# Optimization experiments

Hardware: AMD Instinct MI355X
Metric: run time of the kernel (lower is better)

Reference implementation:

```python
import jax, jax.numpy as jnp
from jax import lax
import numpy as np

C = 768      # embed_dim
H = 8        # num_heads
SR = 2       # sr_ratio
EPS = 1e-5


def setup_inputs() -> dict:
    key = jax.random.key(0)
    ks = jax.random.split(key, 8)
    B, n = 1, 24
    N = n ** 3  # 13824
    s = 0.02
    x = jax.random.normal(ks[0], (B, N, C), jnp.float32)
    wq = jax.random.normal(ks[1], (C, C), jnp.float32) * s          # query (no bias)
    wkv = jax.random.normal(ks[2], (C, 2 * C), jnp.float32) * s     # key_value (no bias)
    sr_w = jax.random.normal(ks[3], (C, C, SR, SR, SR), jnp.float32) * s  # Conv3d OIDHW
    sr_b = jax.random.normal(ks[4], (C,), jnp.float32) * s
    ln_g = jnp.ones((C,), jnp.float32)
    ln_b = jnp.zeros((C,), jnp.float32)
    proj_w = jax.random.normal(ks[5], (C, C), jnp.float32) * s
    proj_b = jax.random.normal(ks[6], (C,), jnp.float32) * s
    return {"x": x, "wq": wq, "wkv": wkv, "sr_w": sr_w, "sr_b": sr_b,
            "ln_g": ln_g, "ln_b": ln_b, "proj_w": proj_w, "proj_b": proj_b}


def reference(x, wq, wkv, sr_w, sr_b, ln_g, ln_b, proj_w, proj_b):
    B, N, Cdim = x.shape
    d = Cdim // H
    n = round(N ** (1.0 / 3.0))
    # q: [B,H,N,d]
    q = (x @ wq).reshape(B, N, H, d).transpose(0, 2, 1, 3)
    # spatial reduction: conv3d with kernel=stride=SR
    x_ = x.transpose(0, 2, 1).reshape(B, Cdim, n, n, n)
    x_ = lax.conv_general_dilated(x_, sr_w, (SR, SR, SR), 'VALID',
                                  dimension_numbers=('NCDHW', 'OIDHW', 'NCDHW'))
    x_ = x_ + sr_b[None, :, None, None, None]
    x_ = x_.reshape(B, Cdim, -1).transpose(0, 2, 1)  # [B, N', C]
    mu = x_.mean(-1, keepdims=True)
    var = x_.var(-1, keepdims=True)
    x_ = (x_ - mu) / jnp.sqrt(var + EPS) * ln_g + ln_b
    # kv: [2,B,H,N',d]
    kv = (x_ @ wkv).reshape(B, -1, 2, H, d).transpose(2, 0, 3, 1, 4)
    k, v = kv[0], kv[1]
    # NOTE: original scales by sqrt(num_heads), not sqrt(head_dim) -- kept faithfully.
    scores = jnp.einsum('bhqd,bhkd->bhqk', q, k) / jnp.sqrt(jnp.float32(H))
    probs = jax.nn.softmax(scores, axis=-1)
    out = jnp.einsum('bhqk,bhkd->bhqd', probs, v)
    out = out.transpose(0, 2, 1, 3).reshape(B, N, Cdim)
    return out @ proj_w + proj_b
```

## Files before the change

kernel.cpp:

```cpp
#include <hip/hip_runtime.h>
#include <hip/hip_bf16.h>

typedef __hip_bfloat16 bf16;
typedef unsigned short u16;

#define CD 768
#define HH 8
#define HD 96
#define NT 13824
#define NR 1728
#define KCONV 6144

typedef __attribute__((ext_vector_type(8))) __bf16 bf16x8;
typedef __attribute__((ext_vector_type(8))) unsigned short us8;
typedef __attribute__((ext_vector_type(4))) unsigned short us4;
typedef __attribute__((ext_vector_type(4))) float floatx4;

#define OFF_XB   0L
#define OFF_Q    21233664L
#define OFF_XR   42467328L
#define OFF_XLN  47775744L
#define OFF_WQT  50429952L
#define OFF_WKVT 51609600L
#define OFF_PRJT 53968896L
#define OFF_SRWR 55148544L
#define OFF_PRB  64587264L
#define OFF_FLAG 64588800L

__device__ __forceinline__ float b2f(bf16 v) { return __bfloat162float(v); }
__device__ __forceinline__ floatx4 mfma16(bf16x8 a, bf16x8 b, floatx4 c) {
    return __builtin_amdgcn_mfma_f32_16x16x32_bf16(a, b, c, 0, 0, 0);
}
__device__ __forceinline__ u16 f2bf_bits(float x) {
    return __builtin_bit_cast(u16, __float2bfloat16(x));
}
__device__ __forceinline__ float ldin(const void* p, long i, int bf) {
    return bf ? b2f(((const bf16*)p)[i]) : ((const float*)p)[i];
}

__global__ void detect_kernel(const unsigned short* __restrict__ g, int* __restrict__ flag) {
    *flag = (g[0] == 0x3F80) ? 1 : 0;
}

__global__ __launch_bounds__(256) void cvt_kernel(
    const void* __restrict__ src, bf16* __restrict__ dst, long nchunk,
    const int* __restrict__ flagp)
{
    const int bf = *flagp;
    long c = (long)blockIdx.x * 256 + threadIdx.x;
    if (c >= nchunk) return;
    if (bf) {
        ((us8*)dst)[c] = ((const us8*)src)[c];
    } else {
        const float* s = (const float*)src + c * 8;
        us8 o;
#pragma unroll
        for (int j = 0; j < 8; ++j) o[j] = f2bf_bits(s[j]);
        ((us8*)dst)[c] = o;
    }
}

__global__ __launch_bounds__(256) void trans_kernel(
    const void* __restrict__ src, bf16* __restrict__ dst, int R, int Cc,
    const int* __restrict__ flagp)
{
    const int bf = *flagp;
    __shared__ float tile[32][33];
    const int tx = threadIdx.x & 31, ty = threadIdx.x >> 5;
    const int bx = blockIdx.x * 32, by = blockIdx.y * 32;
#pragma unroll
    for (int rr = 0; rr < 4; ++rr)
        tile[ty + rr * 8][tx] = ldin(src, (long)(by + ty + rr * 8) * Cc + bx + tx, bf);
    __syncthreads();
#pragma unroll
    for (int rr = 0; rr < 4; ++rr)
        dst[(long)(bx + ty + rr * 8) * R + by + tx] =
            __float2bfloat16(tile[tx][ty + rr * 8]);
}

__global__ __launch_bounds__(256) void reorder_srw_kernel(
    const void* __restrict__ src, bf16* __restrict__ dst,
    const int* __restrict__ flagp)
{
    const int bf = *flagp;
    const long total = 768L * 6144;
    for (long e = (long)blockIdx.x * 256 + threadIdx.x; e < total;
         e += (long)gridDim.x * 256) {
        long o = e / 6144;
        int rem = (int)(e - o * 6144);
        int tap = rem / 768, i = rem - tap * 768;
        dst[e] = __float2bfloat16(ldin(src, o * 6144 + i * 8 + tap, bf));
    }
}

template <bool GATHER, bool BIAS, int DST, int SPLITK, bool PRESCALE>
__global__ __launch_bounds__(256) void gemm_mfma(
    const bf16* __restrict__ A, const bf16* __restrict__ Bt,
    const bf16* __restrict__ bias, void* __restrict__ C, bf16* __restrict__ C2,
    int M, int N, int K, const int* __restrict__ flagp)
{
    const int bf = (DST == 0) ? *flagp : 0;
    __shared__ u16 Al[128][40];
    __shared__ u16 Bl[128][40];
    const int tid  = threadIdx.x;
    const int wave = tid >> 6, lane = tid & 63;
    const int l15  = lane & 15, quad = lane >> 4;
    const int m0 = blockIdx.y * 128, n0 = blockIdx.x * 128;
    const int mw = (wave & 1) * 64, nw = (wave >> 1) * 64;
    const int srow = tid >> 1, koff = (tid & 1) * 16;

    const int mclamp = min(m0 + srow, M - 1);
    int tokbase = 0;
    if (GATHER) {
        int zo = mclamp / 144, yo = (mclamp / 12) % 12, xo = mclamp % 12;
        tokbase = zo * 1152 + yo * 48 + xo * 2;
    }
    const long arow_off = (long)mclamp * K;
    const long brow_off = (long)(n0 + srow) * K;

    floatx4 acc[4][4];
#pragma unroll
    for (int mi = 0; mi < 4; ++mi)
#pragma unroll
        for (int ni = 0; ni < 4; ++ni) acc[mi][ni] = (floatx4){0.f, 0.f, 0.f, 0.f};

    const int ksteps = K >> 5;
    const int kchunk = ksteps / SPLITK;
    const int kb0 = (SPLITK > 1) ? blockIdx.z * kchunk : 0;
    for (int kb = kb0; kb < kb0 + kchunk; ++kb) {
        const bf16* asrc;
        if (GATHER) {
            int kk0 = kb << 5;
            int tap = kk0 / 768;
            int i0  = kk0 - tap * 768 + koff;
            int tok = tokbase + (tap >> 2) * 576 + ((tap >> 1) & 1) * 24 + (tap & 1);
            asrc = A + (long)tok * 768 + i0;
        } else {
            asrc = A + arow_off + (kb << 5) + koff;
        }
        us8 a0 = *(const us8*)asrc;
        us8 a1 = *(const us8*)(asrc + 8);
        us8 b0 = *(const us8*)(Bt + brow_off + (kb << 5) + koff);
        us8 b1 = *(const us8*)(Bt + brow_off + (kb << 5) + koff + 8);
        __syncthreads();
        *(us8*)&Al[srow][koff]     = a0;
        *(us8*)&Al[srow][koff + 8] = a1;
        *(us8*)&Bl[srow][koff]     = b0;
        *(us8*)&Bl[srow][koff + 8] = b1;
        __syncthreads();

        bf16x8 af[4], bfr[4];
#pragma unroll
        for (int mi = 0; mi < 4; ++mi)
            af[mi] = *(const bf16x8*)&Al[mw + mi * 16 + l15][quad * 8];
#pragma unroll
        for (int ni = 0; ni < 4; ++ni)
            bfr[ni] = *(const bf16x8*)&Bl[nw + ni * 16 + l15][quad * 8];
#pragma unroll
        for (int mi = 0; mi < 4; ++mi)
#pragma unroll
            for (int ni = 0; ni < 4; ++ni)
                acc[mi][ni] = mfma16(af[mi], bfr[ni], acc[mi][ni]);
    }

#pragma unroll
    for (int mi = 0; mi < 4; ++mi) {
        int rowb = m0 + mw + mi * 16 + quad * 4;
#pragma unroll
        for (int ni = 0; ni < 4; ++ni) {
            int col = n0 + nw + ni * 16 + l15;
            float bv = BIAS ? b2f(bias[col]) : 0.f;
#pragma unroll
            for (int r = 0; r < 4; ++r) {
                int row = rowb + r;
                if (row < M) {
                    float v = acc[mi][ni][r] + bv;
                    if (PRESCALE) v *= 0.35355339059327373f;
                    long idx = (long)row * N + col;
                    if (DST == 2)      ((float*)C)[idx] = v;
                    else if (DST == 1) ((bf16*)C)[idx] = __float2bfloat16(v);
                    else if (DST == 3) {
                        if (col < 768) ((bf16*)C)[(long)row * 768 + col] = __float2bfloat16(v);
                        else           C2[(long)(col - 768) * NR + row] = __float2bfloat16(v);
                    } else if (DST == 4) {
                        atomicAdd((float*)C + idx, v);
                    } else {
                        if (bf) ((bf16*)C)[idx] = __float2bfloat16(v);
                        else    ((float*)C)[idx] = v;
                    }
                }
            }
        }
    }
}

__global__ __launch_bounds__(256) void ln_kernel(
    const float* __restrict__ Xr, const void* __restrict__ srb,
    const void* __restrict__ g, const void* __restrict__ b,
    bf16* __restrict__ Xln, const int* __restrict__ flagp)
{
    const int bf = *flagp;
    __shared__ float red[256];
    __shared__ float mu_s, rs_s;
    const int t = blockIdx.x, tid = threadIdx.x;
    const float* row = Xr + (long)t * CD;
    float v0 = row[tid]       + ldin(srb, tid, bf);
    float v1 = row[tid + 256] + ldin(srb, tid + 256, bf);
    float v2 = row[tid + 512] + ldin(srb, tid + 512, bf);
    red[tid] = v0 + v1 + v2;
    __syncthreads();
    for (int off = 128; off; off >>= 1) {
        if (tid < off) red[tid] += red[tid + off];
        __syncthreads();
    }
    if (tid == 0) mu_s = red[0] * (1.0f / CD);
    __syncthreads();
    float mu = mu_s;
    float d0 = v0 - mu, d1 = v1 - mu, d2 = v2 - mu;
    red[tid] = d0 * d0 + d1 * d1 + d2 * d2;
    __syncthreads();
    for (int off = 128; off; off >>= 1) {
        if (tid < off) red[tid] += red[tid + off];
        __syncthreads();
    }
    if (tid == 0) rs_s = rsqrtf(red[0] * (1.0f / CD) + 1e-5f);
    __syncthreads();
    float rs = rs_s;
    bf16* orow = Xln + (long)t * CD;
    orow[tid]       = __float2bfloat16(d0 * rs * ldin(g, tid, bf)       + ldin(b, tid, bf));
    orow[tid + 256] = __float2bfloat16(d1 * rs * ldin(g, tid + 256, bf) + ldin(b, tid + 256, bf));
    orow[tid + 512] = __float2bfloat16(d2 * rs * ldin(g, tid + 512, bf) + ldin(b, tid + 512, bf));
}

__global__ __launch_bounds__(256) void attn_mfma_kernel(
    const bf16* __restrict__ Qg, const bf16* __restrict__ Kg,
    const bf16* __restrict__ VTg, bf16* __restrict__ Og)
{
    __shared__ u16 Ks[64][104];
    __shared__ u16 Vt[96][72];
    __shared__ u16 PT[4][32][72];

    const int tid  = threadIdx.x;
    const int wave = tid >> 6;
    const int lane = tid & 63;
    const int l15  = lane & 15;
    const int quad = lane >> 4;

    const int lin  = blockIdx.y * 108 + blockIdx.x;
    const int nid  = (lin & 7) * 108 + (lin >> 3);
    const int h    = nid / 108;
    const int qblk = nid - h * 108;
    const int q0   = qblk * 128 + wave * 32;

    bf16x8 bq[2][3];
#pragma unroll
    for (int qc = 0; qc < 2; ++qc)
#pragma unroll
        for (int kc = 0; kc < 3; ++kc)
            bq[qc][kc] = *(const bf16x8*)(Qg + (long)(q0 + qc * 16 + l15) * CD
                                          + h * HD + kc * 32 + quad * 8);

    floatx4 o[2][6];
    float lp[2] = {0.f, 0.f};
#pragma unroll
    for (int qc = 0; qc < 2; ++qc)
#pragma unroll
        for (int dc = 0; dc < 6; ++dc) o[qc][dc] = (floatx4){0.f, 0.f, 0.f, 0.f};

    const int stok = tid >> 2;
    const int dseg = (tid & 3) * 24;
    const int vdim = tid >> 3;
    const int vt8  = (tid & 7) << 3;
    const u16* kbase = (const u16*)Kg + (long)stok * 768 + h * HD + dseg;
    const u16* vbase = (const u16*)VTg + (long)(h * HD + vdim) * NR + vt8;

    us8 kreg[3], vreg[3];
#pragma unroll
    for (int s = 0; s < 3; ++s) kreg[s] = *(const us8*)(kbase + s * 8);
#pragma unroll
    for (int i = 0; i < 3; ++i) vreg[i] = *(const us8*)(vbase + (long)i * 32 * NR);

    for (int kt = 0; kt < NR; kt += 64) {
        __syncthreads();
#pragma unroll
        for (int s = 0; s < 3; ++s) *(us8*)&Ks[stok][dseg + s * 8] = kreg[s];
#pragma unroll
        for (int i = 0; i < 3; ++i) *(us8*)&Vt[vdim + i * 32][vt8] = vreg[i];
        __syncthreads();

        if (kt + 64 < NR) {
            const u16* k2 = kbase + (long)(kt + 64) * 768;
            const u16* v2 = vbase + (kt + 64);
#pragma unroll
            for (int s = 0; s < 3; ++s) kreg[s] = *(const us8*)(k2 + s * 8);
#pragma unroll
            for (int i = 0; i < 3; ++i) vreg[i] = *(const us8*)(v2 + (long)i * 32 * NR);
        }

#pragma unroll
        for (int tc = 0; tc < 4; ++tc) {
            bf16x8 ak[3];
#pragma unroll
            for (int kc = 0; kc < 3; ++kc)
                ak[kc] = *(const bf16x8*)&Ks[tc * 16 + l15][kc * 32 + quad * 8];
#pragma unroll
            for (int qc = 0; qc < 2; ++qc) {
                floatx4 acc = {0.f, 0.f, 0.f, 0.f};
#pragma unroll
                for (int kc = 0; kc < 3; ++kc) acc = mfma16(ak[kc], bq[qc][kc], acc);
                float e0 = __expf(acc[0]), e1 = __expf(acc[1]);
                float e2 = __expf(acc[2]), e3 = __expf(acc[3]);
                lp[qc] += (e0 + e1) + (e2 + e3);
                us4 p4;
                p4[0] = f2bf_bits(e0); p4[1] = f2bf_bits(e1);
                p4[2] = f2bf_bits(e2); p4[3] = f2bf_bits(e3);
                *(us4*)&PT[wave][qc * 16 + l15][tc * 16 + quad * 4] = p4;
            }
        }

#pragma unroll
        for (int ks = 0; ks < 2; ++ks) {
            bf16x8 ap[2];
#pragma unroll
            for (int qc = 0; qc < 2; ++qc)
                ap[qc] = *(const bf16x8*)&PT[wave][qc * 16 + l15][ks * 32 + quad * 8];
#pragma unroll
            for (int dc = 0; dc < 6; ++dc) {
                bf16x8 bv = *(const bf16x8*)&Vt[dc * 16 + l15][ks * 32 + quad * 8];
#pragma unroll
                for (int qc = 0; qc < 2; ++qc)
                    o[qc][dc] = mfma16(ap[qc], bv, o[qc][dc]);
            }
        }
    }

#pragma unroll
    for (int qc = 0; qc < 2; ++qc) {
        float ls = lp[qc];
        ls += __shfl_xor(ls, 16);
        ls += __shfl_xor(ls, 32);
        float inv = 1.0f / ls;
#pragma unroll
        for (int r = 0; r < 4; ++r) {
            float invr = __shfl(inv, quad * 4 + r, 16);
            int row = q0 + qc * 16 + quad * 4 + r;
#pragma unroll
            for (int dc = 0; dc < 6; ++dc)
                Og[(long)row * CD + h * HD + dc * 16 + l15] =
                    __float2bfloat16(o[qc][dc][r] * invr);
        }
    }
}

extern "C" void kernel_launch(void* const* d_in, const int* in_sizes, int n_in,
                              void* d_out, int out_size, void* d_ws, size_t ws_size,
                              hipStream_t stream) {
    const void* x      = d_in[0];
    const void* wq     = d_in[1];
    const void* wkv    = d_in[2];
    const void* sr_w   = d_in[3];
    const void* sr_b   = d_in[4];
    const void* ln_g   = d_in[5];
    const void* ln_b   = d_in[6];
    const void* proj_w = d_in[7];
    const void* proj_b = d_in[8];

    char* ws = (char*)d_ws;
    bf16*  xb    = (bf16*)(ws + OFF_XB);
    bf16*  O     = (bf16*)(ws + OFF_XB);
    bf16*  Q     = (bf16*)(ws + OFF_Q);
    float* Xr    = (float*)(ws + OFF_XR);
    bf16*  Kg    = (bf16*)(ws + OFF_XR);
    bf16*  VTg   = (bf16*)(ws + OFF_XR + 2654208);
    bf16*  Xln   = (bf16*)(ws + OFF_XLN);
    bf16*  wqT   = (bf16*)(ws + OFF_WQT);
    bf16*  wkvT  = (bf16*)(ws + OFF_WKVT);
    bf16*  prjT  = (bf16*)(ws + OFF_PRJT);
    bf16*  srwR  = (bf16*)(ws + OFF_SRWR);
    bf16*  prbB  = (bf16*)(ws + OFF_PRB);
    int*   flag  = (int*)(ws + OFF_FLAG);

    detect_kernel<<<1, 1, 0, stream>>>((const unsigned short*)ln_g, flag);
    cvt_kernel<<<5184, 256, 0, stream>>>(x, xb, (long)NT * CD / 8, flag);
    trans_kernel<<<dim3(24, 24), 256, 0, stream>>>(wq, wqT, CD, CD, flag);
    trans_kernel<<<dim3(48, 24), 256, 0, stream>>>(wkv, wkvT, CD, 1536, flag);
    trans_kernel<<<dim3(24, 24), 256, 0, stream>>>(proj_w, prjT, CD, CD, flag);
    reorder_srw_kernel<<<4608, 256, 0, stream>>>(sr_w, srwR, flag);
    cvt_kernel<<<1, 256, 0, stream>>>(proj_b, prbB, CD / 8, flag);

    hipMemsetAsync(Xr, 0, (long)NR * CD * 4, stream);
    gemm_mfma<true, false, 4, 4, false><<<dim3(6, 14, 4), 256, 0, stream>>>(
        xb, srwR, nullptr, Xr, nullptr, NR, CD, KCONV, flag);
    ln_kernel<<<NR, 256, 0, stream>>>(Xr, sr_b, ln_g, ln_b, Xln, flag);
    gemm_mfma<false, false, 3, 1, false><<<dim3(12, 14), 256, 0, stream>>>(
        Xln, wkvT, nullptr, Kg, VTg, NR, 1536, CD, flag);
    gemm_mfma<false, false, 1, 1, true><<<dim3(6, 108), 256, 0, stream>>>(
        xb, wqT, nullptr, Q, nullptr, NT, CD, CD, flag);
    attn_mfma_kernel<<<dim3(NT / 128, HH), 256, 0, stream>>>(Q, Kg, VTg, O);
    gemm_mfma<false, true, 0, 1, false><<<dim3(6, 108), 256, 0, stream>>>(
        O, prjT, prbB, d_out, nullptr, NT, CD, CD, flag);
}
```

Baseline: 423.2 us.

## Prefetch next GEMM k-tile into registers and double attention query tile per wave

In the shared GEMM kernel, the global loads for the next k-step are now issued right after the LDS store barrier, so their latency overlaps the MFMA work on the current tile. In the attention kernel, each wave now handles 64 queries instead of 32 (256 per block), so every K/V tile staged in LDS is reused across twice as many queries and the grid is halved. This raises register and LDS use per block (launch bounds request 2 blocks per SM), which may lower occupancy and the number of blocks available to fill the device.

```diff
diff --git a/kernel.cpp b/kernel.cpp
--- a/kernel.cpp
+++ b/kernel.cpp
@@ -127,27 +127,51 @@
     const int ksteps = K >> 5;
     const int kchunk = ksteps / SPLITK;
     const int kb0 = (SPLITK > 1) ? blockIdx.z * kchunk : 0;
-    for (int kb = kb0; kb < kb0 + kchunk; ++kb) {
+    const int kbend = kb0 + kchunk;
+
+    us8 a0, a1, b0, b1;
+    {
         const bf16* asrc;
         if (GATHER) {
-            int kk0 = kb << 5;
+            int kk0 = kb0 << 5;
             int tap = kk0 / 768;
             int i0  = kk0 - tap * 768 + koff;
             int tok = tokbase + (tap >> 2) * 576 + ((tap >> 1) & 1) * 24 + (tap & 1);
             asrc = A + (long)tok * 768 + i0;
         } else {
-            asrc = A + arow_off + (kb << 5) + koff;
-        }
-        us8 a0 = *(const us8*)asrc;
-        us8 a1 = *(const us8*)(asrc + 8);
-        us8 b0 = *(const us8*)(Bt + brow_off + (kb << 5) + koff);
-        us8 b1 = *(const us8*)(Bt + brow_off + (kb << 5) + koff + 8);
+            asrc = A + arow_off + (kb0 << 5) + koff;
+        }
+        a0 = *(const us8*)asrc;
+        a1 = *(const us8*)(asrc + 8);
+        b0 = *(const us8*)(Bt + brow_off + (kb0 << 5) + koff);
+        b1 = *(const us8*)(Bt + brow_off + (kb0 << 5) + koff + 8);
+    }
+
+    for (int kb = kb0; kb < kbend; ++kb) {
         __syncthreads();
         *(us8*)&Al[srow][koff]     = a0;
         *(us8*)&Al[srow][koff + 8] = a1;
         *(us8*)&Bl[srow][koff]     = b0;
         *(us8*)&Bl[srow][koff + 8] = b1;
         __syncthreads();
+
+        if (kb + 1 < kbend) {
+            const int kn = kb + 1;
+            const bf16* asrc;
+            if (GATHER) {
+                int kk0 = kn << 5;
+                int tap = kk0 / 768;
+                int i0  = kk0 - tap * 768 + koff;
+                int tok = tokbase + (tap >> 2) * 576 + ((tap >> 1) & 1) * 24 + (tap & 1);
+                asrc = A + (long)tok * 768 + i0;
+            } else {
+                asrc = A + arow_off + (kn << 5) + koff;
+            }
+            a0 = *(const us8*)asrc;
+            a1 = *(const us8*)(asrc + 8);
+            b0 = *(const us8*)(Bt + brow_off + (kn << 5) + koff);
+            b1 = *(const us8*)(Bt + brow_off + (kn << 5) + koff + 8);
+        }
 
         bf16x8 af[4], bfr[4];
 #pragma unroll
@@ -232,13 +256,13 @@
     orow[tid + 512] = __float2bfloat16(d2 * rs * ldin(g, tid + 512, bf) + ldin(b, tid + 512, bf));
 }
 
-__global__ __launch_bounds__(256) void attn_mfma_kernel(
+__global__ __launch_bounds__(256, 2) void attn_mfma_kernel(
     const bf16* __restrict__ Qg, const bf16* __restrict__ Kg,
     const bf16* __restrict__ VTg, bf16* __restrict__ Og)
 {
     __shared__ u16 Ks[64][104];
     __shared__ u16 Vt[96][72];
-    __shared__ u16 PT[4][32][72];
+    __shared__ u16 PT[4][64][72];
 
     const int tid  = threadIdx.x;
     const int wave = tid >> 6;
@@ -246,24 +270,24 @@
     const int l15  = lane & 15;
     const int quad = lane >> 4;
 
-    const int lin  = blockIdx.y * 108 + blockIdx.x;
-    const int nid  = (lin & 7) * 108 + (lin >> 3);
-    const int h    = nid / 108;
-    const int qblk = nid - h * 108;
-    const int q0   = qblk * 128 + wave * 32;
-
-    bf16x8 bq[2][3];
-#pragma unroll
-    for (int qc = 0; qc < 2; ++qc)
+    const int lin  = blockIdx.y * 54 + blockIdx.x;
+    const int nid  = (lin & 7) * 54 + (lin >> 3);
+    const int h    = nid / 54;
+    const int qblk = nid - h * 54;
+    const int q0   = qblk * 256 + wave * 64;
+
+    bf16x8 bq[4][3];
+#pragma unroll
+    for (int qc = 0; qc < 4; ++qc)
 #pragma unroll
         for (int kc = 0; kc < 3; ++kc)
             bq[qc][kc] = *(const bf16x8*)(Qg + (long)(q0 + qc * 16 + l15) * CD
                                           + h * HD + kc * 32 + quad * 8);
 
-    floatx4 o[2][6];
-    float lp[2] = {0.f, 0.f};
-#pragma unroll
-    for (int qc = 0; qc < 2; ++qc)
+    floatx4 o[4][6];
+    float lp[4] = {0.f, 0.f, 0.f, 0.f};
+#pragma unroll
+    for (int qc = 0; qc < 4; ++qc)
 #pragma unroll
         for (int dc = 0; dc < 6; ++dc) o[qc][dc] = (floatx4){0.f, 0.f, 0.f, 0.f};
 
@@ -304,7 +328,7 @@
             for (int kc = 0; kc < 3; ++kc)
                 ak[kc] = *(const bf16x8*)&Ks[tc * 16 + l15][kc * 32 + quad * 8];
 #pragma unroll
-            for (int qc = 0; qc < 2; ++qc) {
+            for (int qc = 0; qc < 4; ++qc) {
                 floatx4 acc = {0.f, 0.f, 0.f, 0.f};
 #pragma unroll
                 for (int kc = 0; kc < 3; ++kc) acc = mfma16(ak[kc], bq[qc][kc], acc);
@@ -320,22 +344,22 @@
 
 #pragma unroll
         for (int ks = 0; ks < 2; ++ks) {
-            bf16x8 ap[2];
-#pragma unroll
-            for (int qc = 0; qc < 2; ++qc)
+            bf16x8 ap[4];
+#pragma unroll
+            for (int qc = 0; qc < 4; ++qc)
                 ap[qc] = *(const bf16x8*)&PT[wave][qc * 16 + l15][ks * 32 + quad * 8];
 #pragma unroll
             for (int dc = 0; dc < 6; ++dc) {
                 bf16x8 bv = *(const bf16x8*)&Vt[dc * 16 + l15][ks * 32 + quad * 8];
 #pragma unroll
-                for (int qc = 0; qc < 2; ++qc)
+                for (int qc = 0; qc < 4; ++qc)
                     o[qc][dc] = mfma16(ap[qc], bv, o[qc][dc]);
             }
         }
     }
 
 #pragma unroll
-    for (int qc = 0; qc < 2; ++qc) {
+    for (int qc = 0; qc < 4; ++qc) {
         float ls = lp[qc];
         ls += __shfl_xor(ls, 16);
         ls += __shfl_xor(ls, 32);
@@ -396,7 +420,7 @@
         Xln, wkvT, nullptr, Kg, VTg, NR, 1536, CD, flag);
     gemm_mfma<false, false, 1, 1, true><<<dim3(6, 108), 256, 0, stream>>>(
         xb, wqT, nullptr, Q, nullptr, NT, CD, CD, flag);
-    attn_mfma_kernel<<<dim3(NT / 128, HH), 256, 0, stream>>>(Q, Kg, VTg, O);
+    attn_mfma_kernel<<<dim3(NT / 256, HH), 256, 0, stream>>>(Q, Kg, VTg, O);
     gemm_mfma<false, true, 0, 1, false><<<dim3(6, 108), 256, 0, stream>>>(
         O, prjT, prbB, d_out, nullptr, NT, CD, CD, flag);
 }
```

After: 406.1 us. -4.0%, faster.
